# Performance work log

Hardware: AMD Instinct MI355X
Metric: run time of the kernel (lower is better)

## Reference

```python
import jax, jax.numpy as jnp
import numpy as np

B, C, D, T = 64, 1024, 32, 32
F4 = C // 4
GLOBAL_MARGIN = 0.2
MAX_VIOLATION = True
EPS = 1e-8


def setup_inputs() -> dict:
    key = jax.random.key(0)
    k = jax.random.split(key, 8)
    videos = jax.random.normal(k[0], (B, C, D, T), jnp.float32)
    sentences = jax.random.normal(k[1], (B, C), jnp.float32)
    lam = jnp.full((1,), 0.3, jnp.float32)
    mask = jnp.ones((B, D, T), jnp.int32)
    iou_maps = jax.random.uniform(k[2], (D * T, D * T), dtype=jnp.float32)
    lim = float(np.sqrt(6.0 / (C + F4)))  # xavier_uniform for Linear(C, C//4)
    W_v = jax.random.uniform(k[3], (4, C, F4), jnp.float32, -lim, lim)
    b_v = jnp.zeros((4, F4), jnp.float32)
    W_s = jax.random.uniform(k[4], (4, C, F4), jnp.float32, -lim, lim)
    b_s = jnp.zeros((4, F4), jnp.float32)
    return dict(videos=videos, sentences=sentences, lam=lam, mask=mask,
                iou_maps=iou_maps, valid_num=50,
                W_v=W_v, b_v=b_v, W_s=W_s, b_s=b_s)


def _forward(videos, sentences, W_v, b_v, W_s, b_s, lam, mask, iou_maps, valid_num):
    b, c, d, t = videos.shape
    # per-sample channel-mean centering
    videos = videos - jnp.mean(videos, axis=1, keepdims=True)
    sentences = sentences - jnp.mean(sentences, axis=1, keepdims=True)
    # 4-way linear projections, concatenated back along channel dim
    v = jnp.transpose(videos, (0, 2, 3, 1))                      # [b,d,t,c]
    v_cat = (jnp.einsum('bdtc,kcf->bkfdt', v, W_v)
             + b_v[None, :, :, None, None]).reshape(b, c, d, t)  # [b,c,d,t]
    s_cat = (jnp.einsum('bc,kcf->bkf', sentences, W_s) + b_s[None]).reshape(b, c)
    # cosine similarity over channel dim, vectorized over the batch loop
    vn = v_cat / jnp.maximum(jnp.linalg.norm(v_cat, axis=1, keepdims=True), EPS)
    sn = s_cat / jnp.maximum(jnp.linalg.norm(s_cat, axis=1, keepdims=True), EPS)
    sim = jnp.einsum('bcdt,sc->sbdt', vn, sn)                    # [s,b,d,t]
    sim = jnp.where(mask[None] == 0, -jnp.inf, sim)
    positive_map = sim[jnp.arange(b), jnp.arange(b)]             # [b,d,t]
    # top-k proposals + soft-NMS suppression (get_video_score_nms)
    flat = sim.reshape(b, b, d * t)
    vals, idx = jax.lax.top_k(flat, valid_num)                   # [s,b,v]
    iou_sub = iou_maps[idx[..., :, None], idx[..., None, :]]     # [s,b,v,v]
    tril = jnp.tril(jnp.ones((valid_num, valid_num), vals.dtype), -1)
    penalty = jnp.einsum('sblk,lk->sbk', iou_sub * iou_sub, tril)
    w = jnp.exp(-penalty / lam[0])                               # gaussian soft-NMS weight
    scores = jnp.mean(vals * w, axis=-1)                         # [s,b]
    # margin-based contrastive loss on the b x b score matrix
    diag = jnp.diagonal(scores)
    cost_s = jnp.clip(GLOBAL_MARGIN + scores - diag[:, None], 0.0)
    cost_im = jnp.clip(GLOBAL_MARGIN + scores - diag[None, :], 0.0)
    eye = jnp.eye(b, dtype=bool)
    cost_s = jnp.where(eye, 0.0, cost_s)
    cost_im = jnp.where(eye, 0.0, cost_im)
    if MAX_VIOLATION:
        cost_s = cost_s.max(axis=1)
        cost_im = cost_im.max(axis=0)
    loss = cost_s.sum() / b + cost_im.sum() / b
    return loss, positive_map


def reference(videos, sentences, lam, mask, iou_maps, valid_num, W_v, b_v, W_s, b_s):
    return _forward(videos, sentences, W_v, b_v, W_s, b_s, lam, mask, iou_maps, valid_num)
```

## Files before the change

### kernel.cpp

```cpp
#include <hip/hip_runtime.h>
#include <cstdint>
#include <cstddef>

#define CDIM  1024
#define DTDIM 1024
#define MDIM  65536
#define BDIM  64
#define VNUM  50

typedef __attribute__((ext_vector_type(8))) short bf16x8;
typedef __attribute__((ext_vector_type(4))) float f32x4;

__device__ __forceinline__ float bf2f(unsigned int u16) {
  return __uint_as_float(u16 << 16);
}
__device__ __forceinline__ unsigned short f2bf(float x) {
  unsigned int u = __float_as_uint(x);
  u += 0x7fffu + ((u >> 16) & 1u);
  return (unsigned short)(u >> 16);
}

__device__ __forceinline__ void gload16(const void* g, void* l) {
  __builtin_amdgcn_global_load_lds((const __attribute__((address_space(1))) void*)g,
                                   (__attribute__((address_space(3))) void*)l,
                                   16, 0, 0);
}

__global__ void k_transpose_videos(const float* __restrict__ vid,
                                   unsigned short* __restrict__ At,
                                   float* __restrict__ vsums) {
  __shared__ float t[32][33];
  const int tx = threadIdx.x & 31, ty = threadIdx.x >> 5;
  const int dt0 = blockIdx.x * 32, c0 = blockIdx.y * 32, b = blockIdx.z;
  const float* src = vid + ((size_t)b * CDIM + c0) * DTDIM + dt0;
#pragma unroll
  for (int i = 0; i < 4; i++) {
    const int cl = ty + i * 8;
    t[cl][tx] = src[(size_t)cl * DTDIM + tx];
  }
  __syncthreads();
  unsigned short* dst = At + ((size_t)b * DTDIM + dt0) * CDIM + c0;
#pragma unroll
  for (int i = 0; i < 4; i++) {
    const int dl = ty + i * 8;
    const float val = t[tx][dl];
    dst[(size_t)dl * CDIM + tx] = f2bf(val);
    float s = val;
    s += __shfl_xor(s, 1);  s += __shfl_xor(s, 2);
    s += __shfl_xor(s, 4);  s += __shfl_xor(s, 8);
    s += __shfl_xor(s, 16);
    if (tx == 0) atomicAdd(&vsums[(size_t)b * DTDIM + dt0 + dl], s);
  }
}

__global__ void k_transpose_W(const float* __restrict__ W,
                              unsigned short* __restrict__ Wt) {
  __shared__ float t[32][33];
  const int tx = threadIdx.x & 31, ty = threadIdx.x >> 5;
  const int f0 = blockIdx.x * 32, c0 = blockIdx.y * 32, kb = blockIdx.z;
  const float* src = W + ((size_t)kb * CDIM + c0) * 256 + f0;
#pragma unroll
  for (int i = 0; i < 4; i++) {
    const int cl = ty + i * 8;
    t[cl][tx] = src[(size_t)cl * 256 + tx];
  }
  __syncthreads();
  unsigned short* dst = Wt + ((size_t)(kb * 256 + f0)) * CDIM + c0;
#pragma unroll
  for (int i = 0; i < 4; i++) {
    const int fl = ty + i * 8;
    dst[(size_t)fl * CDIM + tx] = f2bf(t[tx][fl]);
  }
}

__global__ void k_row_sums(const unsigned short* __restrict__ A,
                           float* __restrict__ out, int nrows) {
  const int wave = threadIdx.x >> 6, lane = threadIdx.x & 63;
  const int row = blockIdx.x * 4 + wave;
  if (row >= nrows) return;
  const unsigned short* r = A + (size_t)row * 1024;
  float s = 0.f;
#pragma unroll
  for (int h = 0; h < 2; h++) {
    const uint4 u = *reinterpret_cast<const uint4*>(r + h * 512 + lane * 8);
    s += bf2f(u.x & 0xffffu) + bf2f(u.x >> 16);
    s += bf2f(u.y & 0xffffu) + bf2f(u.y >> 16);
    s += bf2f(u.z & 0xffffu) + bf2f(u.z >> 16);
    s += bf2f(u.w & 0xffffu) + bf2f(u.w >> 16);
  }
#pragma unroll
  for (int o = 32; o; o >>= 1) s += __shfl_down(s, o);
  if (lane == 0) out[row] = s;
}

__global__ void k_scat(const float* __restrict__ sent, const float* __restrict__ Ws,
                       const float* __restrict__ bs, unsigned short* __restrict__ scat,
                       float* __restrict__ snorm2) {
  const int s = blockIdx.x, j = blockIdx.y, tid = threadIdx.x;
  __shared__ float sc[1024];
  __shared__ float red[4];
  float p = 0.f;
#pragma unroll
  for (int q = 0; q < 4; q++) {
    const float x = sent[(size_t)s * 1024 + tid + q * 256];
    sc[tid + q * 256] = x;
    p += x;
  }
#pragma unroll
  for (int o = 32; o; o >>= 1) p += __shfl_down(p, o);
  const int wave = tid >> 6, lane = tid & 63;
  if (lane == 0) red[wave] = p;
  __syncthreads();
  const float mean = (red[0] + red[1] + red[2] + red[3]) * (1.f / 1024.f);
  float acc = 0.f;
  const float* W = Ws + ((size_t)j * 1024) * 256 + tid;
  for (int c = 0; c < 1024; c++) acc += (sc[c] - mean) * W[(size_t)c * 256];
  const int n = j * 256 + tid;
  const float val = acc + bs[n];
  scat[(size_t)s * 1024 + n] = f2bf(val);
  float v2 = val * val;
#pragma unroll
  for (int o = 32; o; o >>= 1) v2 += __shfl_down(v2, o);
  if (lane == 0) atomicAdd(&snorm2[s], v2);
}

__global__ void k_gemm1(const unsigned short* __restrict__ At,
                        const unsigned short* __restrict__ Wt,
                        const float* __restrict__ vsums, const float* __restrict__ csW,
                        const float* __restrict__ bv,
                        unsigned short* __restrict__ vcat, float* __restrict__ vnorm2) {
  __shared__ alignas(16) unsigned short sA[128 * 32];
  __shared__ alignas(16) unsigned short sB[128 * 32];
  const int tid = threadIdx.x;
  const int wave = tid >> 6, lane = tid & 63;
  const int quad = lane >> 4, l16 = lane & 15;
  const int m0 = blockIdx.x * 128, n0 = blockIdx.y * 128;
  const int wm = (wave & 1) * 64, wn = (wave >> 1) * 64;

  f32x4 acc[4][4];
#pragma unroll
  for (int i = 0; i < 4; i++)
#pragma unroll
    for (int j = 0; j < 4; j++) acc[i][j] = f32x4{0.f, 0.f, 0.f, 0.f};

  const int rowA0 = (wave * 2 + 0) * 16 + (lane >> 2);
  const int rowA1 = (wave * 2 + 1) * 16 + (lane >> 2);
  const int kk = (lane & 3) * 8;
  const unsigned short* gA0 = At + (size_t)(m0 + rowA0) * CDIM + kk;
  const unsigned short* gA1 = At + (size_t)(m0 + rowA1) * CDIM + kk;
  const unsigned short* gB0 = Wt + (size_t)(n0 + rowA0) * CDIM + kk;
  const unsigned short* gB1 = Wt + (size_t)(n0 + rowA1) * CDIM + kk;
  unsigned short* lA0 = &sA[(wave * 2 + 0) * 512];
  unsigned short* lA1 = &sA[(wave * 2 + 1) * 512];
  unsigned short* lB0 = &sB[(wave * 2 + 0) * 512];
  unsigned short* lB1 = &sB[(wave * 2 + 1) * 512];

  for (int kt = 0; kt < 32; ++kt) {
    const int koff = kt * 32;
    gload16(gA0 + koff, lA0);
    gload16(gA1 + koff, lA1);
    gload16(gB0 + koff, lB0);
    gload16(gB1 + koff, lB1);
    __syncthreads();
    bf16x8 aF[4], bF[4];
#pragma unroll
    for (int i = 0; i < 4; i++)
      aF[i] = *reinterpret_cast<const bf16x8*>(&sA[(wm + i * 16 + l16) * 32 + quad * 8]);
#pragma unroll
    for (int j = 0; j < 4; j++)
      bF[j] = *reinterpret_cast<const bf16x8*>(&sB[(wn + j * 16 + l16) * 32 + quad * 8]);
#pragma unroll
    for (int i = 0; i < 4; i++)
#pragma unroll
      for (int j = 0; j < 4; j++)
        acc[i][j] = __builtin_amdgcn_mfma_f32_16x16x32_bf16(aF[i], bF[j], acc[i][j], 0, 0, 0);
    __syncthreads();
  }

  const float inv1024 = 1.f / 1024.f;
#pragma unroll
  for (int i = 0; i < 4; i++) {
    const int rbase = m0 + wm + i * 16 + quad * 4;
    const float4 vs = *reinterpret_cast<const float4*>(&vsums[rbase]);
    const float mu[4] = {vs.x * inv1024, vs.y * inv1024, vs.z * inv1024, vs.w * inv1024};
    float ss[4] = {0.f, 0.f, 0.f, 0.f};
#pragma unroll
    for (int j = 0; j < 4; j++) {
      const int col = n0 + wn + j * 16 + l16;
      const float cs = csW[col];
      const float bb = bv[col];
#pragma unroll
      for (int r = 0; r < 4; r++) {
        const float val = acc[i][j][r] - mu[r] * cs + bb;
        vcat[(size_t)(rbase + r) * CDIM + col] = f2bf(val);
        ss[r] += val * val;
      }
    }
#pragma unroll
    for (int r = 0; r < 4; r++) {
      float v = ss[r];
      v += __shfl_xor(v, 1); v += __shfl_xor(v, 2);
      v += __shfl_xor(v, 4); v += __shfl_xor(v, 8);
      if (l16 == 0) atomicAdd(&vnorm2[rbase + r], v);
    }
  }
}

__global__ void k_gemm2(const unsigned short* __restrict__ scat,
                        const unsigned short* __restrict__ vcat,
                        const float* __restrict__ snorm2, const float* __restrict__ vnorm2,
                        const int* __restrict__ mask,
                        float* __restrict__ sim, float* __restrict__ pm) {
  __shared__ alignas(16) unsigned short sS[64 * 32];
  __shared__ alignas(16) unsigned short sV[128 * 32];
  const int tid = threadIdx.x;
  const int wave = tid >> 6, lane = tid & 63;
  const int quad = lane >> 4, l16 = lane & 15;
  const int m0 = blockIdx.x * 128;

  f32x4 acc[4][2];
#pragma unroll
  for (int i = 0; i < 4; i++)
#pragma unroll
    for (int j = 0; j < 2; j++) acc[i][j] = f32x4{0.f, 0.f, 0.f, 0.f};

  const int rS = wave * 16 + (lane >> 2);
  const int rV0 = (wave * 2 + 0) * 16 + (lane >> 2);
  const int rV1 = (wave * 2 + 1) * 16 + (lane >> 2);
  const int kk = (lane & 3) * 8;
  const unsigned short* gS = scat + (size_t)rS * CDIM + kk;
  const unsigned short* gV0 = vcat + (size_t)(m0 + rV0) * CDIM + kk;
  const unsigned short* gV1 = vcat + (size_t)(m0 + rV1) * CDIM + kk;
  unsigned short* lS = &sS[wave * 512];
  unsigned short* lV0 = &sV[(wave * 2 + 0) * 512];
  unsigned short* lV1 = &sV[(wave * 2 + 1) * 512];

  for (int kt = 0; kt < 32; ++kt) {
    const int koff = kt * 32;
    gload16(gS + koff, lS);
    gload16(gV0 + koff, lV0);
    gload16(gV1 + koff, lV1);
    __syncthreads();
    bf16x8 aF[4], bF[2];
#pragma unroll
    for (int i = 0; i < 4; i++)
      aF[i] = *reinterpret_cast<const bf16x8*>(&sS[(i * 16 + l16) * 32 + quad * 8]);
#pragma unroll
    for (int j = 0; j < 2; j++)
      bF[j] = *reinterpret_cast<const bf16x8*>(&sV[(wave * 32 + j * 16 + l16) * 32 + quad * 8]);
#pragma unroll
    for (int i = 0; i < 4; i++)
#pragma unroll
      for (int j = 0; j < 2; j++)
        acc[i][j] = __builtin_amdgcn_mfma_f32_16x16x32_bf16(aF[i], bF[j], acc[i][j], 0, 0, 0);
    __syncthreads();
  }

  const int b0 = m0 >> 10;
#pragma unroll
  for (int j = 0; j < 2; j++) {
    const int m = m0 + wave * 32 + j * 16 + l16;
    const float vn = fmaxf(sqrtf(vnorm2[m]), 1e-8f);
    const int mk = mask[m];
#pragma unroll
    for (int i = 0; i < 4; i++) {
#pragma unroll
      for (int r = 0; r < 4; r++) {
        const int s = i * 16 + quad * 4 + r;
        const float sn = fmaxf(sqrtf(snorm2[s]), 1e-8f);
        float val = acc[i][j][r] / (vn * sn);
        if (mk == 0) val = -__builtin_inff();
        sim[(size_t)s * MDIM + m] = val;
        if (s == b0) pm[m] = val;
      }
    }
  }
}

__global__ void k_topk(const float* __restrict__ sim, const float* __restrict__ iou,
                       const float* __restrict__ lam, float* __restrict__ scores) {
  const int wave = threadIdx.x >> 6, lane = threadIdx.x & 63;
  const int sb = blockIdx.x * 4 + wave;
  const int s = sb >> 6, b = sb & 63;
  __shared__ float tvs[4][VNUM];
  __shared__ int tis[4][VNUM];

  const float* row = sim + (size_t)s * MDIM + (size_t)b * 1024;
  float v[16];
#pragma unroll
  for (int j = 0; j < 16; j++) v[j] = row[j * 64 + lane];

  for (int k = 0; k < VNUM; k++) {
    float bv = v[0]; int bj = 0;
#pragma unroll
    for (int j = 1; j < 16; j++)
      if (v[j] > bv) { bv = v[j]; bj = j; }
    int bidx = bj * 64 + lane;
#pragma unroll
    for (int o = 1; o < 64; o <<= 1) {
      const float ov = __shfl_xor(bv, o);
      const int oi = __shfl_xor(bidx, o);
      if (ov > bv || (ov == bv && oi < bidx)) { bv = ov; bidx = oi; }
    }
    if (lane == 0) { tvs[wave][k] = bv; tis[wave][k] = bidx; }
    const int wj = bidx >> 6;
    const bool mine = (bidx & 63) == lane;
#pragma unroll
    for (int j = 0; j < 16; j++)
      if (mine && wj == j) v[j] = -__builtin_inff();
  }
  __syncthreads();

  float contrib = 0.f;
  if (lane < VNUM) {
    const int myidx = tis[wave][lane];
    float pen = 0.f;
    for (int l = lane + 1; l < VNUM; l++) {
      const float u = iou[(size_t)tis[wave][l] * 1024 + myidx];
      pen += u * u;
    }
    contrib = tvs[wave][lane] * expf(-pen / lam[0]);
  }
#pragma unroll
  for (int o = 32; o; o >>= 1) contrib += __shfl_down(contrib, o);
  if (lane == 0) scores[s * 64 + b] = contrib * (1.f / VNUM);
}

__global__ void k_loss(const float* __restrict__ scores, float* __restrict__ out) {
  __shared__ float S[64 * 64];
  __shared__ float diag[64];
  __shared__ float rmax[64], cmax[64];
  const int tid = threadIdx.x;
#pragma unroll
  for (int q = 0; q < 16; q++) S[tid + q * 256] = scores[tid + q * 256];
  __syncthreads();
  if (tid < 64) diag[tid] = S[tid * 64 + tid];
  __syncthreads();
  if (tid < 64) {
    float rm = 0.f, cm = 0.f;
    for (int x = 0; x < 64; x++) {
      if (x != tid) {
        const float cs = 0.2f + S[tid * 64 + x] - diag[tid];
        rm = fmaxf(rm, fmaxf(cs, 0.f));
        const float ci = 0.2f + S[x * 64 + tid] - diag[tid];
        cm = fmaxf(cm, fmaxf(ci, 0.f));
      }
    }
    rmax[tid] = rm; cmax[tid] = cm;
  }
  __syncthreads();
  if (tid == 0) {
    float L = 0.f;
    for (int t = 0; t < 64; t++) L += rmax[t] + cmax[t];
    out[0] = L * (1.f / 64.f);
  }
}

extern "C" void kernel_launch(void* const* d_in, const int* in_sizes, int n_in,
                              void* d_out, int out_size, void* d_ws, size_t ws_size,
                              hipStream_t stream) {
  (void)in_sizes; (void)n_in; (void)out_size; (void)ws_size;
  const float* videos = (const float*)d_in[0];
  const float* sent   = (const float*)d_in[1];
  const float* lam    = (const float*)d_in[2];
  const int*   mask   = (const int*)d_in[3];
  const float* iou    = (const float*)d_in[4];
  const float* W_v    = (const float*)d_in[6];
  const float* b_v    = (const float*)d_in[7];
  const float* W_s    = (const float*)d_in[8];
  const float* b_s    = (const float*)d_in[9];
  float* out = (float*)d_out;

  char* ws = (char*)d_ws;
  unsigned short* At   = (unsigned short*)(ws + 0);
  unsigned short* vcat = (unsigned short*)(ws + 134217728);
  float* sim           = (float*)(ws + 268435456);
  unsigned short* Wt   = (unsigned short*)(ws + 285212672);
  unsigned short* scat = (unsigned short*)(ws + 287309824);
  float* vsums         = (float*)(ws + 287440896);
  float* vnorm2        = (float*)(ws + 287703040);
  float* snorm2        = (float*)(ws + 287965184);
  float* csW           = (float*)(ws + 287965440);
  float* scores        = (float*)(ws + 287969536);

  hipMemsetAsync(vsums, 0, 262144 + 262144 + 256, stream);

  k_transpose_videos<<<dim3(32, 32, 64), 256, 0, stream>>>(videos, At, vsums);
  k_transpose_W<<<dim3(8, 32, 4), 256, 0, stream>>>(W_v, Wt);
  k_row_sums<<<256, 256, 0, stream>>>(Wt, csW, 1024);
  k_scat<<<dim3(64, 4), 256, 0, stream>>>(sent, W_s, b_s, scat, snorm2);
  k_gemm1<<<dim3(512, 8), 256, 0, stream>>>(At, Wt, vsums, csW, b_v, vcat, vnorm2);
  k_gemm2<<<dim3(512), 256, 0, stream>>>(scat, vcat, snorm2, vnorm2, mask, sim, out + 1);
  k_topk<<<dim3(1024), 256, 0, stream>>>(sim, iou, lam, scores);
  k_loss<<<1, 256, 0, stream>>>(scores, out);
}
```

Baseline: 816.7 us.

## Widen video transpose tiles, swizzle GEMM LDS layout, and group GEMM1 block order

The video transpose now uses 64x64 tiles with float4 global reads and packed bf16x2 writes, which cuts the number of narrow memory transactions and halves the row-sum atomics. Both GEMM kernels XOR-swizzle the k-chunk position inside LDS rows, on the global-to-LDS load side and the fragment-read side, to reduce bank conflicts. GEMM1 switches to a 1D grid whose block order groups 8 M-tiles with all 8 N-tiles so A tiles are reused in cache. The added risks are index-mapping errors in the swizzle and more LDS per transpose block.

```diff
diff --git a/kernel.cpp b/kernel.cpp
--- a/kernel.cpp
+++ b/kernel.cpp
@@ -29,27 +29,33 @@
 __global__ void k_transpose_videos(const float* __restrict__ vid,
                                    unsigned short* __restrict__ At,
                                    float* __restrict__ vsums) {
-  __shared__ float t[32][33];
-  const int tx = threadIdx.x & 31, ty = threadIdx.x >> 5;
-  const int dt0 = blockIdx.x * 32, c0 = blockIdx.y * 32, b = blockIdx.z;
+  __shared__ float t[64][65];
+  const int tid = threadIdx.x;
+  const int dt0 = blockIdx.x * 64, c0 = blockIdx.y * 64, b = blockIdx.z;
+  const int lc = tid >> 4;
+  const int l4 = (tid & 15) * 4;
   const float* src = vid + ((size_t)b * CDIM + c0) * DTDIM + dt0;
 #pragma unroll
-  for (int i = 0; i < 4; i++) {
-    const int cl = ty + i * 8;
-    t[cl][tx] = src[(size_t)cl * DTDIM + tx];
-  }
-  __syncthreads();
-  unsigned short* dst = At + ((size_t)b * DTDIM + dt0) * CDIM + c0;
-#pragma unroll
-  for (int i = 0; i < 4; i++) {
-    const int dl = ty + i * 8;
-    const float val = t[tx][dl];
-    dst[(size_t)dl * CDIM + tx] = f2bf(val);
-    float s = val;
-    s += __shfl_xor(s, 1);  s += __shfl_xor(s, 2);
-    s += __shfl_xor(s, 4);  s += __shfl_xor(s, 8);
-    s += __shfl_xor(s, 16);
-    if (tx == 0) atomicAdd(&vsums[(size_t)b * DTDIM + dt0 + dl], s);
+  for (int p = 0; p < 4; p++) {
+    const int c = p * 16 + lc;
+    const float4 f = *reinterpret_cast<const float4*>(&src[(size_t)c * DTDIM + l4]);
+    t[c][l4 + 0] = f.x; t[c][l4 + 1] = f.y; t[c][l4 + 2] = f.z; t[c][l4 + 3] = f.w;
+  }
+  __syncthreads();
+  const int dr = tid >> 5;
+  const int cl = tid & 31;
+  unsigned int* dstbase = reinterpret_cast<unsigned int*>(
+      At + ((size_t)(b * DTDIM + dt0)) * CDIM + c0);
+#pragma unroll
+  for (int p = 0; p < 8; p++) {
+    const int dt = p * 8 + dr;
+    const float a0 = t[2 * cl][dt], a1 = t[2 * cl + 1][dt];
+    const unsigned int u = (unsigned int)f2bf(a0) | ((unsigned int)f2bf(a1) << 16);
+    dstbase[(size_t)dt * 512 + cl] = u;
+    float s = a0 + a1;
+    s += __shfl_xor(s, 1);  s += __shfl_xor(s, 2);  s += __shfl_xor(s, 4);
+    s += __shfl_xor(s, 8);  s += __shfl_xor(s, 16);
+    if (cl == 0) atomicAdd(&vsums[(size_t)b * DTDIM + dt0 + dt], s);
   }
 }
 
@@ -134,7 +140,9 @@
   const int tid = threadIdx.x;
   const int wave = tid >> 6, lane = tid & 63;
   const int quad = lane >> 4, l16 = lane & 15;
-  const int m0 = blockIdx.x * 128, n0 = blockIdx.y * 128;
+  const int id = blockIdx.x;
+  const int m0 = (((id >> 6) << 3) + (id & 7)) * 128;
+  const int n0 = ((id >> 3) & 7) * 128;
   const int wm = (wave & 1) * 64, wn = (wave >> 1) * 64;
 
   f32x4 acc[4][4];
@@ -143,9 +151,10 @@
 #pragma unroll
     for (int j = 0; j < 4; j++) acc[i][j] = f32x4{0.f, 0.f, 0.f, 0.f};
 
-  const int rowA0 = (wave * 2 + 0) * 16 + (lane >> 2);
-  const int rowA1 = (wave * 2 + 1) * 16 + (lane >> 2);
-  const int kk = (lane & 3) * 8;
+  const int r = lane >> 2;
+  const int kk = (((lane & 3) ^ ((r >> 1) & 3)) * 8);
+  const int rowA0 = (wave * 2 + 0) * 16 + r;
+  const int rowA1 = (wave * 2 + 1) * 16 + r;
   const unsigned short* gA0 = At + (size_t)(m0 + rowA0) * CDIM + kk;
   const unsigned short* gA1 = At + (size_t)(m0 + rowA1) * CDIM + kk;
   const unsigned short* gB0 = Wt + (size_t)(n0 + rowA0) * CDIM + kk;
@@ -155,6 +164,8 @@
   unsigned short* lB0 = &sB[(wave * 2 + 0) * 512];
   unsigned short* lB1 = &sB[(wave * 2 + 1) * 512];
 
+  const int sw = (l16 >> 1) & 3;
+
   for (int kt = 0; kt < 32; ++kt) {
     const int koff = kt * 32;
     gload16(gA0 + koff, lA0);
@@ -165,10 +176,12 @@
     bf16x8 aF[4], bF[4];
 #pragma unroll
     for (int i = 0; i < 4; i++)
-      aF[i] = *reinterpret_cast<const bf16x8*>(&sA[(wm + i * 16 + l16) * 32 + quad * 8]);
+      aF[i] = *reinterpret_cast<const bf16x8*>(
+          &sA[(wm + i * 16 + l16) * 32 + ((quad ^ sw) * 8)]);
 #pragma unroll
     for (int j = 0; j < 4; j++)
-      bF[j] = *reinterpret_cast<const bf16x8*>(&sB[(wn + j * 16 + l16) * 32 + quad * 8]);
+      bF[j] = *reinterpret_cast<const bf16x8*>(
+          &sB[(wn + j * 16 + l16) * 32 + ((quad ^ sw) * 8)]);
 #pragma unroll
     for (int i = 0; i < 4; i++)
 #pragma unroll
@@ -190,18 +203,18 @@
       const float cs = csW[col];
       const float bb = bv[col];
 #pragma unroll
-      for (int r = 0; r < 4; r++) {
-        const float val = acc[i][j][r] - mu[r] * cs + bb;
-        vcat[(size_t)(rbase + r) * CDIM + col] = f2bf(val);
-        ss[r] += val * val;
+      for (int rr = 0; rr < 4; rr++) {
+        const float val = acc[i][j][rr] - mu[rr] * cs + bb;
+        vcat[(size_t)(rbase + rr) * CDIM + col] = f2bf(val);
+        ss[rr] += val * val;
       }
     }
 #pragma unroll
-    for (int r = 0; r < 4; r++) {
-      float v = ss[r];
+    for (int rr = 0; rr < 4; rr++) {
+      float v = ss[rr];
       v += __shfl_xor(v, 1); v += __shfl_xor(v, 2);
       v += __shfl_xor(v, 4); v += __shfl_xor(v, 8);
-      if (l16 == 0) atomicAdd(&vnorm2[rbase + r], v);
+      if (l16 == 0) atomicAdd(&vnorm2[rbase + rr], v);
     }
   }
 }
@@ -224,16 +237,19 @@
 #pragma unroll
     for (int j = 0; j < 2; j++) acc[i][j] = f32x4{0.f, 0.f, 0.f, 0.f};
 
-  const int rS = wave * 16 + (lane >> 2);
-  const int rV0 = (wave * 2 + 0) * 16 + (lane >> 2);
-  const int rV1 = (wave * 2 + 1) * 16 + (lane >> 2);
-  const int kk = (lane & 3) * 8;
+  const int r = lane >> 2;
+  const int kk = (((lane & 3) ^ ((r >> 1) & 3)) * 8);
+  const int rS = wave * 16 + r;
+  const int rV0 = (wave * 2 + 0) * 16 + r;
+  const int rV1 = (wave * 2 + 1) * 16 + r;
   const unsigned short* gS = scat + (size_t)rS * CDIM + kk;
   const unsigned short* gV0 = vcat + (size_t)(m0 + rV0) * CDIM + kk;
   const unsigned short* gV1 = vcat + (size_t)(m0 + rV1) * CDIM + kk;
   unsigned short* lS = &sS[wave * 512];
   unsigned short* lV0 = &sV[(wave * 2 + 0) * 512];
   unsigned short* lV1 = &sV[(wave * 2 + 1) * 512];
+
+  const int sw = (l16 >> 1) & 3;
 
   for (int kt = 0; kt < 32; ++kt) {
     const int koff = kt * 32;
@@ -244,10 +260,12 @@
     bf16x8 aF[4], bF[2];
 #pragma unroll
     for (int i = 0; i < 4; i++)
-      aF[i] = *reinterpret_cast<const bf16x8*>(&sS[(i * 16 + l16) * 32 + quad * 8]);
+      aF[i] = *reinterpret_cast<const bf16x8*>(
+          &sS[(i * 16 + l16) * 32 + ((quad ^ sw) * 8)]);
 #pragma unroll
     for (int j = 0; j < 2; j++)
-      bF[j] = *reinterpret_cast<const bf16x8*>(&sV[(wave * 32 + j * 16 + l16) * 32 + quad * 8]);
+      bF[j] = *reinterpret_cast<const bf16x8*>(
+          &sV[(wave * 32 + j * 16 + l16) * 32 + ((quad ^ sw) * 8)]);
 #pragma unroll
     for (int i = 0; i < 4; i++)
 #pragma unroll
@@ -265,10 +283,10 @@
 #pragma unroll
     for (int i = 0; i < 4; i++) {
 #pragma unroll
-      for (int r = 0; r < 4; r++) {
-        const int s = i * 16 + quad * 4 + r;
+      for (int rr = 0; rr < 4; rr++) {
+        const int s = i * 16 + quad * 4 + rr;
         const float sn = fmaxf(sqrtf(snorm2[s]), 1e-8f);
-        float val = acc[i][j][r] / (vn * sn);
+        float val = acc[i][j][rr] / (vn * sn);
         if (mk == 0) val = -__builtin_inff();
         sim[(size_t)s * MDIM + m] = val;
         if (s == b0) pm[m] = val;
@@ -385,11 +403,11 @@
 
   hipMemsetAsync(vsums, 0, 262144 + 262144 + 256, stream);
 
-  k_transpose_videos<<<dim3(32, 32, 64), 256, 0, stream>>>(videos, At, vsums);
+  k_transpose_videos<<<dim3(16, 16, 64), 256, 0, stream>>>(videos, At, vsums);
   k_transpose_W<<<dim3(8, 32, 4), 256, 0, stream>>>(W_v, Wt);
   k_row_sums<<<256, 256, 0, stream>>>(Wt, csW, 1024);
   k_scat<<<dim3(64, 4), 256, 0, stream>>>(sent, W_s, b_s, scat, snorm2);
-  k_gemm1<<<dim3(512, 8), 256, 0, stream>>>(At, Wt, vsums, csW, b_v, vcat, vnorm2);
+  k_gemm1<<<dim3(4096), 256, 0, stream>>>(At, Wt, vsums, csW, b_v, vcat, vnorm2);
   k_gemm2<<<dim3(512), 256, 0, stream>>>(scat, vcat, snorm2, vnorm2, mask, sim, out + 1);
   k_topk<<<dim3(1024), 256, 0, stream>>>(sim, iou, lam, scores);
   k_loss<<<1, 256, 0, stream>>>(scores, out);
```

New measurement: 742.9 us. 1.1x faster.
